# Kernel tuning notes

Measured on AMD Instinct MI355X. Metric: run time of the kernel, lower is better.

The kernel has to match this reference:

```python
import jax, jax.numpy as jnp
import numpy as np

N = 100_000   # nodes
E = 1_600_000 # edges
G, H1, H2, Z = 64, 64, 64, 32


def _w(k, o, i):
    return jax.random.normal(k, (o, i), jnp.float32) * (1.0 / np.sqrt(i))


def setup_inputs() -> dict:
    key = jax.random.key(0)
    ks = jax.random.split(key, 16)
    inp = {
        "x": jax.random.normal(ks[0], (N, G), jnp.float32),
        "edge_src": jax.random.randint(ks[1], (E,), 0, N, jnp.int32),
        "edge_dst": jax.random.randint(ks[2], (E,), 0, N, jnp.int32),
        "eps": jax.random.normal(ks[3], (N, Z), jnp.float32),
        "W1": _w(ks[4], H1, G),  "b1": jnp.zeros((H1,), jnp.float32),
        "W2": _w(ks[5], H2, H1), "b2": jnp.zeros((H2,), jnp.float32),
        "W31": _w(ks[6], Z, H2), "b31": jnp.zeros((Z,), jnp.float32),
        "W32": _w(ks[7], Z, H2), "b32": jnp.zeros((Z,), jnp.float32),
        "W4": _w(ks[8], H2, Z),  "b4": jnp.zeros((H2,), jnp.float32),
        "W5": _w(ks[9], H1, H2), "b5": jnp.zeros((H1,), jnp.float32),
        "W6": _w(ks[10], G, H1), "b6": jnp.zeros((G,), jnp.float32),
    }
    return inp


def _gcn(h, W, b, act, src, dst, norm):
    # message: h_src * norm_src, gathered per edge  [E, d]
    m = (h * norm)[src]
    # reduce: sum over incoming edges, scaled by norm_dst  [N, d]
    agg = jax.ops.segment_sum(m, dst, num_segments=N) * norm
    # node apply: linear + activation
    return act(agg @ W.T + b)


def reference(x, edge_src, edge_dst, eps,
              W1, b1, W2, b2, W31, b31, W32, b32, W4, b4, W5, b5, W6, b6):
    # symmetric GCN norm: deg^{-1/2} from in-degree
    deg = jax.ops.segment_sum(jnp.ones((E,), jnp.float32), edge_dst, num_segments=N)
    norm = jax.lax.rsqrt(jnp.maximum(deg, 1.0))[:, None]  # [N,1]

    relu = jax.nn.relu
    ident = lambda h: h

    h = _gcn(x, W1, b1, relu, edge_src, edge_dst, norm)
    h = _gcn(h, W2, b2, relu, edge_src, edge_dst, norm)
    mu = _gcn(h, W31, b31, ident, edge_src, edge_dst, norm)
    log_var = _gcn(h, W32, b32, ident, edge_src, edge_dst, norm)

    z = eps * jnp.exp(0.5 * log_var) + mu

    h = _gcn(z, W4, b4, relu, edge_src, edge_dst, norm)
    h = _gcn(h, W5, b5, relu, edge_src, edge_dst, norm)
    recon = _gcn(h, W6, b6, jax.nn.sigmoid, edge_src, edge_dst, norm)
    return recon, mu, log_var
```

## Files before the change

kernel.cpp:

```cpp
#include <hip/hip_runtime.h>
#include <hip/hip_fp16.h>
#include <math.h>

#define NN 100000
#define NE 1600000
#define NBKT 391
#define CHUNK 8192
#define NB1 ((NE + CHUNK - 1) / CHUNK)
#define QSEG 25000
#define NNP (NN + 8)
#define CAP 5120

typedef _Float16 v8h __attribute__((ext_vector_type(8)));
typedef float v4f __attribute__((ext_vector_type(4)));
typedef unsigned int v4u __attribute__((ext_vector_type(4)));

union H4 { uint2 u; __half2 h[2]; };

__global__ __launch_bounds__(256) void p1_scatter_kernel(const int* __restrict__ src,
                                                         const int* __restrict__ dst,
                                                         int* __restrict__ bcnt,
                                                         int* __restrict__ gpair) {
    __shared__ int h[NBKT], rb[NBKT], hc[NBKT];
    int tid = threadIdx.x;
    for (int b = tid; b < NBKT; b += 256) { h[b] = 0; hc[b] = 0; }
    __syncthreads();
    int e0 = blockIdx.x * CHUNK;
    for (int k = 0; k < CHUNK / 256; ++k) {
        int e = e0 + tid + k * 256;
        if (e < NE) atomicAdd(&h[dst[e] >> 8], 1);
    }
    __syncthreads();
    for (int b = tid; b < NBKT; b += 256)
        rb[b] = h[b] ? atomicAdd(&bcnt[b], h[b]) : 0;
    __syncthreads();
    for (int k = 0; k < CHUNK / 256; ++k) {
        int e = e0 + tid + k * 256;
        if (e < NE) {
            int d = dst[e], s = src[e];
            int b = d >> 8;
            int pos = b * CAP + rb[b] + atomicAdd(&hc[b], 1);
            gpair[pos] = (s << 8) | (d & 255);
        }
    }
}

__global__ __launch_bounds__(256) void p2_place_kernel(const int* __restrict__ gpair,
                                                       const int* __restrict__ bcnt,
                                                       int* __restrict__ csr,
                                                       int* __restrict__ seg,
                                                       float* __restrict__ nrm,
                                                       const float4* __restrict__ x4,
                                                       uint2* __restrict__ xs) {
    __shared__ int cseg[4][256], nexcl[256], sb[4][256], pq[4][256];
    __shared__ float nrmS[256];
    int b = blockIdx.x, tid = threadIdx.x;
    int s0 = b * CAP, s1 = s0 + bcnt[b];
#pragma unroll
    for (int q = 0; q < 4; ++q) { cseg[q][tid] = 0; pq[q][tid] = 0; }
    __syncthreads();
    for (int i = s0 + tid; i < s1; i += 256) {
        int p = gpair[i];
        int l = p & 255;
        int q = (p >> 8) / QSEG;
        atomicAdd(&cseg[q][l], 1);
    }
    __syncthreads();
    int v = cseg[0][tid] + cseg[1][tid] + cseg[2][tid] + cseg[3][tid];
    nexcl[tid] = v;
    __syncthreads();
    for (int off = 1; off < 256; off <<= 1) {
        int t = (tid >= off) ? nexcl[tid - off] : 0;
        __syncthreads();
        nexcl[tid] += t;
        __syncthreads();
    }
    int ex = nexcl[tid] - v;
    int base = s0 + ex;
    int node = (b << 8) + tid;
    int c0 = cseg[0][tid], c1 = cseg[1][tid], c2 = cseg[2][tid];
    float nv = rsqrtf(fmaxf((float)v, 1.0f));
    if (node < NN) {
        seg[0 * NNP + node] = base;
        seg[1 * NNP + node] = base + c0;
        seg[2 * NNP + node] = base + c0 + c1;
        seg[3 * NNP + node] = base + c0 + c1 + c2;
        seg[4 * NNP + node] = base + v;
        nrm[node] = nv;
    }
    nrmS[tid] = nv;
    sb[0][tid] = base;
    sb[1][tid] = base + c0;
    sb[2][tid] = base + c0 + c1;
    sb[3][tid] = base + c0 + c1 + c2;
    __syncthreads();
    for (int i = s0 + tid; i < s1; i += 256) {
        int p = gpair[i];
        int l = p & 255;
        int s = p >> 8;
        int q = s / QSEG;
        int pos = sb[q][l] + atomicAdd(&pq[q][l], 1);
        csr[pos] = s;
    }
    int nbase = b << 8;
    int nvalid = NN - nbase; if (nvalid > 256) nvalid = 256;
    for (int idx = tid; idx < nvalid * 16; idx += 256) {
        int nl = idx >> 4, f = idx & 15;
        float s = nrmS[nl];
        float4 xv = x4[(size_t)(nbase + nl) * 16 + f];
        H4 w;
        w.h[0] = __floats2half2_rn(xv.x * s, xv.y * s);
        w.h[1] = __floats2half2_rn(xv.z * s, xv.w * s);
        xs[(size_t)(nbase + nl) * 16 + f] = w.u;
    }
}

template<int IN, int ACT, bool SCALE, bool DUAL>
__global__ __launch_bounds__(256) void gcn_layer_kernel(
        const __half* __restrict__ h,
        const float* __restrict__ nrm,
        const int* __restrict__ seg,
        const int* __restrict__ csr,
        const float* __restrict__ Wa, const float* __restrict__ ba,
        const float* __restrict__ Wb, const float* __restrict__ bb,
        void* __restrict__ outv, float* __restrict__ out2,
        const float* __restrict__ eps, __half* __restrict__ zbuf) {
    constexpr int MLP = 8;
    constexpr int RL  = IN / 4;
    constexpr int EPI = 64 / RL;
    constexpr int KH  = IN / 32;
    constexpr int AS  = IN + 8;
    constexpr int HS  = 72;
    constexpr int FS  = 68;
    constexpr int MS  = 36;
    constexpr int OUTB = DUAL ? (2 * 32 * MS * 4) : (SCALE ? 32 * HS * 2 : 32 * FS * 4);
    __shared__ __half aggH[32 * AS];
    __shared__ __align__(16) char smem[OUTB];

    int tid = threadIdx.x;
    int wave = tid >> 6, lane = tid & 63;
    int row_slot = lane / RL;
    int f4 = lane % RL;
    int nodeBase = (blockIdx.x * 4 + wave) * MLP;
    const uint2* hp = (const uint2*)h;

    float4 acc[MLP];
#pragma unroll
    for (int i = 0; i < MLP; ++i) acc[i] = make_float4(0.f, 0.f, 0.f, 0.f);

    int cur[MLP];
#pragma unroll
    for (int i = 0; i < MLP; ++i) cur[i] = seg[nodeBase + i];

    for (int q = 0; q < 4; ++q) {
        {
            constexpr int CPR = IN / 8;
            int g = (int)(blockIdx.x >> 3);
            int r0 = q * QSEG + g * 64;
            int rend = (q + 1) * QSEG;
            int r1 = r0 + 64; if (r1 > rend) r1 = rend;
            if (r0 < r1) {
                const v4u* sl = (const v4u*)h + (size_t)r0 * CPR;
                int chunks = (r1 - r0) * CPR;
                unsigned wsum = 0;
                for (int c = tid; c < chunks; c += 256) {
                    v4u tv = sl[c];
                    wsum ^= tv.x ^ tv.y ^ tv.z ^ tv.w;
                }
                asm volatile("" :: "v"(wsum));
            }
        }

        int nxt[MLP];
#pragma unroll
        for (int i = 0; i < MLP; ++i) nxt[i] = seg[(q + 1) * NNP + nodeBase + i];
        int maxd = 0;
#pragma unroll
        for (int i = 0; i < MLP; ++i) maxd = max(maxd, nxt[i] - cur[i]);

        for (int t = 0; t < maxd; t += EPI) {
            int s[MLP]; float m[MLP];
#pragma unroll
            for (int i = 0; i < MLP; ++i) {
                int jj = cur[i] + t + row_slot;
                bool ok = jj < nxt[i];
                s[i] = csr[ok ? jj : 0];
                m[i] = ok ? 1.f : 0.f;
            }
            H4 v[MLP];
#pragma unroll
            for (int i = 0; i < MLP; ++i)
                v[i].u = hp[(size_t)s[i] * RL + f4];
#pragma unroll
            for (int i = 0; i < MLP; ++i) {
                float2 f01 = __half22float2(v[i].h[0]);
                float2 f23 = __half22float2(v[i].h[1]);
                acc[i].x = fmaf(m[i], f01.x, acc[i].x);
                acc[i].y = fmaf(m[i], f01.y, acc[i].y);
                acc[i].z = fmaf(m[i], f23.x, acc[i].z);
                acc[i].w = fmaf(m[i], f23.y, acc[i].w);
            }
        }
#pragma unroll
        for (int i = 0; i < MLP; ++i) cur[i] = nxt[i];
    }

#pragma unroll
    for (int i = 0; i < MLP; ++i) {
        for (int o = RL; o < 64; o <<= 1) {
            acc[i].x += __shfl_xor(acc[i].x, o);
            acc[i].y += __shfl_xor(acc[i].y, o);
            acc[i].z += __shfl_xor(acc[i].z, o);
            acc[i].w += __shfl_xor(acc[i].w, o);
        }
    }

    if (row_slot == 0) {
#pragma unroll
        for (int i = 0; i < MLP; ++i) {
            H4 w;
            w.h[0] = __floats2half2_rn(acc[i].x, acc[i].y);
            w.h[1] = __floats2half2_rn(acc[i].z, acc[i].w);
            *(uint2*)&aggH[(wave * MLP + i) * AS + f4 * 4] = w.u;
        }
    }

    int col = lane & 15, kgrp = lane >> 4;
    v8h Bhi[KH], Blo[KH];
    float bias;
    {
        const float* wrow;
        if (DUAL) wrow = (wave < 2) ? (Wa + (size_t)(wave * 16 + col) * 64)
                                    : (Wb + (size_t)((wave - 2) * 16 + col) * 64);
        else      wrow = Wa + (size_t)(wave * 16 + col) * IN;
        bias = DUAL ? ((wave < 2) ? ba[wave * 16 + col] : bb[(wave - 2) * 16 + col])
                    : ba[wave * 16 + col];
#pragma unroll
        for (int kh = 0; kh < KH; ++kh) {
            const float* wp = wrow + kh * 32 + kgrp * 8;
            float4 w0 = *(const float4*)(wp);
            float4 w1 = *(const float4*)(wp + 4);
            float wv[8] = {w0.x, w0.y, w0.z, w0.w, w1.x, w1.y, w1.z, w1.w};
#pragma unroll
            for (int j = 0; j < 8; ++j) {
                _Float16 hv = (_Float16)wv[j];
                Bhi[kh][j] = hv;
                Blo[kh][j] = (_Float16)(wv[j] - (float)hv);
            }
        }
    }
    __syncthreads();

    v4f dacc[2];
#pragma unroll
    for (int a2 = 0; a2 < 2; ++a2) dacc[a2] = (v4f){0.f, 0.f, 0.f, 0.f};

#pragma unroll
    for (int a2 = 0; a2 < 2; ++a2) {
        int arow = a2 * 16 + col;
#pragma unroll
        for (int kh = 0; kh < KH; ++kh) {
            v8h A = *(const v8h*)&aggH[arow * AS + kh * 32 + kgrp * 8];
            dacc[a2] = __builtin_amdgcn_mfma_f32_16x16x32_f16(A, Bhi[kh], dacc[a2], 0, 0, 0);
            dacc[a2] = __builtin_amdgcn_mfma_f32_16x16x32_f16(A, Blo[kh], dacc[a2], 0, 0, 0);
        }
    }

    float*  smu = (float*)smem;
    float*  slv = smu + 32 * MS;
    __half* sh  = (__half*)smem;
    float*  sf  = (float*)smem;
    size_t gbase = (size_t)blockIdx.x * 32;

#pragma unroll
    for (int a2 = 0; a2 < 2; ++a2) {
#pragma unroll
        for (int r = 0; r < 4; ++r) {
            int lnode = a2 * 16 + kgrp * 4 + r;
            float nv = nrm[gbase + lnode];
            float v = dacc[a2][r] * nv + bias;
            if (ACT == 1) v = fmaxf(v, 0.f);
            if (ACT == 2) v = 1.f / (1.f + expf(-v));
            if (DUAL) {
                if (wave < 2) smu[lnode * MS + wave * 16 + col] = v;
                else          slv[lnode * MS + (wave - 2) * 16 + col] = v;
            } else if (SCALE) {
                sh[lnode * HS + wave * 16 + col] = __float2half(v * nv);
            } else {
                sf[lnode * FS + wave * 16 + col] = v;
            }
        }
    }
    __syncthreads();

    if (DUAL) {
        float* mu_p = (float*)outv;
        for (int idx = tid; idx < 32 * 8; idx += 256) {
            int r = idx >> 3, c = idx & 7;
            v4u v = *(const v4u*)&smu[r * MS + c * 4];
            __builtin_nontemporal_store(v, (v4u*)(mu_p + (gbase + r) * 32) + c);
        }
        for (int idx = tid; idx < 32 * 8; idx += 256) {
            int r = idx >> 3, c = idx & 7;
            v4u v = *(const v4u*)&slv[r * MS + c * 4];
            __builtin_nontemporal_store(v, (v4u*)(out2 + (gbase + r) * 32) + c);
        }
        for (int idx = tid; idx < 32 * 4; idx += 256) {
            int r = idx >> 2, c0 = (idx & 3) * 8;
            size_t node = gbase + r;
            float nv = nrm[node];
            float zv[8];
#pragma unroll
            for (int j = 0; j < 8; ++j) {
                float e  = eps[node * 32 + c0 + j];
                float mv = smu[r * MS + c0 + j];
                float lw = slv[r * MS + c0 + j];
                zv[j] = (e * expf(0.5f * lw) + mv) * nv;
            }
            H4 w0, w1;
            w0.h[0] = __floats2half2_rn(zv[0], zv[1]);
            w0.h[1] = __floats2half2_rn(zv[2], zv[3]);
            w1.h[0] = __floats2half2_rn(zv[4], zv[5]);
            w1.h[1] = __floats2half2_rn(zv[6], zv[7]);
            v4u o16;
            o16.x = w0.u.x; o16.y = w0.u.y; o16.z = w1.u.x; o16.w = w1.u.y;
            __builtin_nontemporal_store(o16, (v4u*)(zbuf + node * 32) + (c0 >> 3));
        }
    } else if (SCALE) {
        __half* hout = (__half*)outv;
        for (int idx = tid; idx < 32 * 8; idx += 256) {
            int r = idx >> 3, c = idx & 7;
            v4u v = *(const v4u*)&sh[r * HS + c * 8];
            __builtin_nontemporal_store(v, (v4u*)(hout + (gbase + r) * 64) + c);
        }
    } else {
        float* fout = (float*)outv;
        for (int idx = tid; idx < 32 * 16; idx += 256) {
            int r = idx >> 4, c = idx & 15;
            v4u v = *(const v4u*)&sf[r * FS + c * 4];
            __builtin_nontemporal_store(v, (v4u*)(fout + (gbase + r) * 64) + c);
        }
    }
}

extern "C" void kernel_launch(void* const* d_in, const int* in_sizes, int n_in,
                              void* d_out, int out_size, void* d_ws, size_t ws_size,
                              hipStream_t stream) {
    const float* x    = (const float*)d_in[0];
    const int*   esrc = (const int*)d_in[1];
    const int*   edst = (const int*)d_in[2];
    const float* eps  = (const float*)d_in[3];
    const float* W1  = (const float*)d_in[4];  const float* b1  = (const float*)d_in[5];
    const float* W2  = (const float*)d_in[6];  const float* b2  = (const float*)d_in[7];
    const float* W31 = (const float*)d_in[8];  const float* b31 = (const float*)d_in[9];
    const float* W32 = (const float*)d_in[10]; const float* b32 = (const float*)d_in[11];
    const float* W4  = (const float*)d_in[12]; const float* b4  = (const float*)d_in[13];
    const float* W5  = (const float*)d_in[14]; const float* b5  = (const float*)d_in[15];
    const float* W6  = (const float*)d_in[16]; const float* b6  = (const float*)d_in[17];

    float* outp  = (float*)d_out;
    float* recon = outp;
    float* mu    = outp + (size_t)NN * 64;
    float* lv    = mu   + (size_t)NN * 32;

    int* wsI       = (int*)d_ws;
    int* bcnt      = wsI;
    int* seg       = bcnt + 392;
    int* csr       = seg + 5 * NNP;
    int* gpair     = csr + NBKT * CAP;
    float* nrm     = (float*)(gpair + NBKT * CAP);
    __half* hA     = (__half*)(nrm + NN);
    __half* hB     = hA + (size_t)NN * 64;

    const int fgrid = NN / 32;

    hipMemsetAsync(bcnt, 0, 392 * sizeof(int), stream);
    p1_scatter_kernel<<<NB1, 256, 0, stream>>>(esrc, edst, bcnt, gpair);
    p2_place_kernel<<<NBKT, 256, 0, stream>>>(gpair, bcnt, csr, seg, nrm,
                                              (const float4*)x, (uint2*)hA);

    gcn_layer_kernel<64, 1, true,  false><<<fgrid, 256, 0, stream>>>(hA, nrm, seg, csr, W1,  b1,  nullptr, nullptr, hB,    nullptr, nullptr, nullptr);
    gcn_layer_kernel<64, 1, true,  false><<<fgrid, 256, 0, stream>>>(hB, nrm, seg, csr, W2,  b2,  nullptr, nullptr, hA,    nullptr, nullptr, nullptr);
    gcn_layer_kernel<64, 0, false, true ><<<fgrid, 256, 0, stream>>>(hA, nrm, seg, csr, W31, b31, W32,     b32,     mu,    lv,      eps,     hB);
    gcn_layer_kernel<32, 1, true,  false><<<fgrid, 256, 0, stream>>>(hB, nrm, seg, csr, W4,  b4,  nullptr, nullptr, hA,    nullptr, nullptr, nullptr);
    gcn_layer_kernel<64, 1, true,  false><<<fgrid, 256, 0, stream>>>(hA, nrm, seg, csr, W5,  b5,  nullptr, nullptr, hB,    nullptr, nullptr, nullptr);
    gcn_layer_kernel<64, 2, false, false><<<fgrid, 256, 0, stream>>>(hB, nrm, seg, csr, W6,  b6,  nullptr, nullptr, recon, nullptr, nullptr, nullptr);
}
```

Before: 593.6 us.

## Split source-node range into 8 segments and drop explicit L2 prefetch

The CSR per destination node is now partitioned into 8 source-range segments instead of 4, so each phase of the gather loop touches a smaller slice of the feature table that should stay resident in cache. The explicit per-block prefetch sweep of each source slice is removed. Doubling the segments adds more per-segment loop iterations with partially filled edge batches, plus more seg array traffic and shared memory in the placement kernel.

```diff
diff --git a/kernel.cpp b/kernel.cpp
--- a/kernel.cpp
+++ b/kernel.cpp
@@ -7,7 +7,8 @@
 #define NBKT 391
 #define CHUNK 8192
 #define NB1 ((NE + CHUNK - 1) / CHUNK)
-#define QSEG 25000
+#define SEGS 8
+#define QSEG 12500
 #define NNP (NN + 8)
 #define CAP 5120
 
@@ -52,12 +53,12 @@
                                                        float* __restrict__ nrm,
                                                        const float4* __restrict__ x4,
                                                        uint2* __restrict__ xs) {
-    __shared__ int cseg[4][256], nexcl[256], sb[4][256], pq[4][256];
+    __shared__ int cseg[SEGS][256], nexcl[256], sb[SEGS][256], pq[SEGS][256];
     __shared__ float nrmS[256];
     int b = blockIdx.x, tid = threadIdx.x;
     int s0 = b * CAP, s1 = s0 + bcnt[b];
 #pragma unroll
-    for (int q = 0; q < 4; ++q) { cseg[q][tid] = 0; pq[q][tid] = 0; }
+    for (int q = 0; q < SEGS; ++q) { cseg[q][tid] = 0; pq[q][tid] = 0; }
     __syncthreads();
     for (int i = s0 + tid; i < s1; i += 256) {
         int p = gpair[i];
@@ -66,7 +67,9 @@
         atomicAdd(&cseg[q][l], 1);
     }
     __syncthreads();
-    int v = cseg[0][tid] + cseg[1][tid] + cseg[2][tid] + cseg[3][tid];
+    int v = 0;
+#pragma unroll
+    for (int q = 0; q < SEGS; ++q) v += cseg[q][tid];
     nexcl[tid] = v;
     __syncthreads();
     for (int off = 1; off < 256; off <<= 1) {
@@ -78,21 +81,18 @@
     int ex = nexcl[tid] - v;
     int base = s0 + ex;
     int node = (b << 8) + tid;
-    int c0 = cseg[0][tid], c1 = cseg[1][tid], c2 = cseg[2][tid];
     float nv = rsqrtf(fmaxf((float)v, 1.0f));
-    if (node < NN) {
-        seg[0 * NNP + node] = base;
-        seg[1 * NNP + node] = base + c0;
-        seg[2 * NNP + node] = base + c0 + c1;
-        seg[3 * NNP + node] = base + c0 + c1 + c2;
-        seg[4 * NNP + node] = base + v;
-        nrm[node] = nv;
+    {
+        int run = base;
+#pragma unroll
+        for (int q = 0; q < SEGS; ++q) {
+            if (node < NN) seg[q * NNP + node] = run;
+            sb[q][tid] = run;
+            run += cseg[q][tid];
+        }
+        if (node < NN) { seg[SEGS * NNP + node] = run; nrm[node] = nv; }
     }
     nrmS[tid] = nv;
-    sb[0][tid] = base;
-    sb[1][tid] = base + c0;
-    sb[2][tid] = base + c0 + c1;
-    sb[3][tid] = base + c0 + c1 + c2;
     __syncthreads();
     for (int i = s0 + tid; i < s1; i += 256) {
         int p = gpair[i];
@@ -152,25 +152,7 @@
 #pragma unroll
     for (int i = 0; i < MLP; ++i) cur[i] = seg[nodeBase + i];
 
-    for (int q = 0; q < 4; ++q) {
-        {
-            constexpr int CPR = IN / 8;
-            int g = (int)(blockIdx.x >> 3);
-            int r0 = q * QSEG + g * 64;
-            int rend = (q + 1) * QSEG;
-            int r1 = r0 + 64; if (r1 > rend) r1 = rend;
-            if (r0 < r1) {
-                const v4u* sl = (const v4u*)h + (size_t)r0 * CPR;
-                int chunks = (r1 - r0) * CPR;
-                unsigned wsum = 0;
-                for (int c = tid; c < chunks; c += 256) {
-                    v4u tv = sl[c];
-                    wsum ^= tv.x ^ tv.y ^ tv.z ^ tv.w;
-                }
-                asm volatile("" :: "v"(wsum));
-            }
-        }
-
+    for (int q = 0; q < SEGS; ++q) {
         int nxt[MLP];
 #pragma unroll
         for (int i = 0; i < MLP; ++i) nxt[i] = seg[(q + 1) * NNP + nodeBase + i];
@@ -366,7 +348,7 @@
     int* wsI       = (int*)d_ws;
     int* bcnt      = wsI;
     int* seg       = bcnt + 392;
-    int* csr       = seg + 5 * NNP;
+    int* csr       = seg + (SEGS + 1) * NNP;
     int* gpair     = csr + NBKT * CAP;
     float* nrm     = (float*)(gpair + NBKT * CAP);
     __half* hA     = (__half*)(nrm + NN);
```

Result: slower. 642.2 us (+8.2%).
